# Kernel tuning notes

Measured on AMD Instinct MI355X. Metric: run time of the kernel, lower is better.

Reference implementation:

```python
import jax, jax.numpy as jnp
import numpy as np

INPUT_DIMS = 512
OUTPUT_DIMS = 512
DEGREE = 7
ALPHA = 1.0


def setup_inputs() -> dict:
    key = jax.random.key(0)
    k1, k2 = jax.random.split(key)
    x = jax.random.normal(k1, (16384, INPUT_DIMS), dtype=jnp.float32)
    std = 1.0 / (INPUT_DIMS * (DEGREE + 1))
    coeffs = jax.random.normal(k2, (INPUT_DIMS, OUTPUT_DIMS, DEGREE + 1), dtype=jnp.float32) * std
    return {"x": x, "gegenbauer_coeffs": coeffs}


def reference(x, gegenbauer_coeffs):
    # x: (B, I) -> tanh squashed into (-1, 1) domain of Gegenbauer polys
    x = jnp.tanh(x.reshape(-1, INPUT_DIMS))
    a = ALPHA
    polys = [jnp.ones_like(x)]
    if DEGREE > 0:
        polys.append(2.0 * a * x)
    # recurrence: C_{n+1} = (2(n+a) x C_n - (n+2a-1) C_{n-1}) / (n+1)
    for n in range(1, DEGREE):
        polys.append((2.0 * (n + a) * x * polys[n] - (n + 2.0 * a - 1.0) * polys[n - 1]) / (n + 1.0))
    g = jnp.stack(polys, axis=-1)  # (B, I, D+1)
    y = jnp.einsum('bid,iod->bo', g, gegenbauer_coeffs)
    return y.reshape(-1, OUTPUT_DIMS)
```

## Files before the change

kernel.cpp:

```cpp
#include <hip/hip_runtime.h>
#include <hip/hip_bf16.h>


#define I_DIM 512
#define O_DIM 512
#define NDEG 8
#define BM 128
#define BN 128
#define IPB 8
#define LSTR 72
#define KITERS (I_DIM / IPB)
#define NTHREADS 256
#define W_ELEMS (I_DIM * O_DIM * NDEG)

typedef __attribute__((ext_vector_type(8))) short s8v;
typedef __attribute__((ext_vector_type(4))) float f32x4;
typedef unsigned short u16;

__device__ __forceinline__ unsigned pack2bf(float a, float b) {
    unsigned ua = __float_as_uint(a), ub = __float_as_uint(b);
    ua += 0x7fffu + ((ua >> 16) & 1u);
    ub += 0x7fffu + ((ub >> 16) & 1u);
    return (ua >> 16) | (ub & 0xffff0000u);
}

__device__ __forceinline__ float fast_tanh(float v) {
    float e = __expf(v + v);
    float r = __builtin_amdgcn_rcpf(e + 1.0f);
    return 1.0f - (r + r);
}

extern "C" __global__ __launch_bounds__(256)
void cvt_w(const float* __restrict__ cf, u16* __restrict__ wbf) {
    const size_t idx = ((size_t)blockIdx.x * 256 + threadIdx.x) * 4;
    const float4 v = *reinterpret_cast<const float4*>(cf + idx);
    unsigned* dst = reinterpret_cast<unsigned*>(wbf + idx);
    dst[0] = pack2bf(v.x, v.y);
    dst[1] = pack2bf(v.z, v.w);
}

template <bool PRECONV>
__global__ __launch_bounds__(NTHREADS, 4)
void gegen_gemm(const float* __restrict__ x,
                const float* __restrict__ cf,
                const u16* __restrict__ wbf,
                float* __restrict__ out)
{
    __shared__ u16 As[BM * LSTR];
    __shared__ u16 Ws[IPB * BN * NDEG];

    const int tid  = threadIdx.x;
    const int lane = tid & 63;
    const int wave = tid >> 6;
    const int fm   = lane & 15;
    const int fq   = lane >> 4;
    const int wr   = (wave >> 1) << 6;
    const int wc   = (wave & 1) << 6;

    const int bm0 = blockIdx.y * BM;
    const int bn0 = blockIdx.x * BN;

    const int ar = tid >> 1;
    const int ai = (tid & 1) << 2;
    const float* xp = x + (size_t)(bm0 + ar) * I_DIM + ai;

    f32x4 acc[4][4];
#pragma unroll
    for (int a = 0; a < 4; ++a)
#pragma unroll
        for (int b = 0; b < 4; ++b)
            acc[a][b] = (f32x4){0.0f, 0.0f, 0.0f, 0.0f};

    for (int it = 0; it < KITERS; ++it) {
        if (PRECONV) {
            const u16* wsrc = wbf + ((size_t)(it * IPB) * O_DIM + bn0) * NDEG;
#pragma unroll
            for (int q = 0; q < 4; ++q) {
                const int c    = wave * 4 + q;
                const int il   = c >> 1;
                const int half = c & 1;
                const u16* src = wsrc + ((size_t)il * O_DIM + half * 64 + lane) * NDEG;
                u16* dst = &Ws[(il * BN + half * 64) * NDEG];
                __builtin_amdgcn_global_load_lds(
                    (const __attribute__((address_space(1))) void*)src,
                    (__attribute__((address_space(3))) void*)dst, 16, 0, 0);
            }
        } else {
#pragma unroll
            for (int jj = 0; jj < 4; ++jj) {
                const int p  = jj * NTHREADS + tid;
                const int il = p >> 7;
                const int o  = p & 127;
                const float* src = cf + ((size_t)(it * IPB + il) * O_DIM + bn0 + o) * NDEG;
                const float4 w0 = reinterpret_cast<const float4*>(src)[0];
                const float4 w1 = reinterpret_cast<const float4*>(src)[1];
                union { s8v s; unsigned u[4]; } pk;
                pk.u[0] = pack2bf(w0.x, w0.y);
                pk.u[1] = pack2bf(w0.z, w0.w);
                pk.u[2] = pack2bf(w1.x, w1.y);
                pk.u[3] = pack2bf(w1.z, w1.w);
                *reinterpret_cast<s8v*>(&Ws[(il * BN + o) * NDEG]) = pk.s;
            }
        }

        {
            const float4 xv = *reinterpret_cast<const float4*>(xp + it * IPB);
            const float vv[4] = {xv.x, xv.y, xv.z, xv.w};
#pragma unroll
            for (int j = 0; j < 4; ++j) {
                const float t  = fast_tanh(vv[j]);
                const float t2 = t + t;
                const float c1 = t2;
                const float c2 = t2 * c1 - 1.0f;
                const float c3 = t2 * c2 - c1;
                const float c4 = t2 * c3 - c2;
                const float c5 = t2 * c4 - c3;
                const float c6 = t2 * c5 - c4;
                const float c7 = t2 * c6 - c5;
                union { s8v s; unsigned u[4]; } pk;
                pk.u[0] = pack2bf(1.0f, c1);
                pk.u[1] = pack2bf(c2, c3);
                pk.u[2] = pack2bf(c4, c5);
                pk.u[3] = pack2bf(c6, c7);
                *reinterpret_cast<s8v*>(&As[ar * LSTR + (ai + j) * NDEG]) = pk.s;
            }
        }
        __syncthreads();

#pragma unroll
        for (int kc = 0; kc < 2; ++kc) {
            s8v afr[4], bfr[4];
#pragma unroll
            for (int tm = 0; tm < 4; ++tm)
                afr[tm] = *reinterpret_cast<const s8v*>(
                    &As[(wr + tm * 16 + fm) * LSTR + kc * 32 + fq * 8]);
#pragma unroll
            for (int tn = 0; tn < 4; ++tn)
                bfr[tn] = *reinterpret_cast<const s8v*>(
                    &Ws[((kc * 4 + fq) * BN + wc + tn * 16 + fm) * NDEG]);
#pragma unroll
            for (int tm = 0; tm < 4; ++tm)
#pragma unroll
                for (int tn = 0; tn < 4; ++tn)
                    acc[tm][tn] = __builtin_amdgcn_mfma_f32_16x16x32_bf16(
                        afr[tm], bfr[tn], acc[tm][tn], 0, 0, 0);
        }
        __syncthreads();
    }

#pragma unroll
    for (int tm = 0; tm < 4; ++tm) {
#pragma unroll
        for (int tn = 0; tn < 4; ++tn) {
            const int row = bm0 + wr + tm * 16 + fq * 4;
            const int col = bn0 + wc + tn * 16 + fm;
#pragma unroll
            for (int r = 0; r < 4; ++r)
                out[(size_t)(row + r) * O_DIM + col] = acc[tm][tn][r];
        }
    }
}

extern "C" void kernel_launch(void* const* d_in, const int* in_sizes, int n_in,
                              void* d_out, int out_size, void* d_ws, size_t ws_size,
                              hipStream_t stream) {
    const float* x  = (const float*)d_in[0];
    const float* cf = (const float*)d_in[1];
    float* out = (float*)d_out;
    const int M = in_sizes[0] / I_DIM;
    dim3 grid(O_DIM / BN, M / BM);
    dim3 block(NTHREADS, 1, 1);

    if (ws_size >= (size_t)W_ELEMS * sizeof(u16)) {
        u16* wbf = (u16*)d_ws;
        cvt_w<<<W_ELEMS / 1024, 256, 0, stream>>>(cf, wbf);
        gegen_gemm<true><<<grid, block, 0, stream>>>(x, cf, wbf, out);
    } else {
        gegen_gemm<false><<<grid, block, 0, stream>>>(x, cf, nullptr, out);
    }
}
```

Baseline: 172.2 us.

## Double-buffer LDS tiles to overlap next-tile loads with MFMA compute

Splits the A and W shared-memory tiles into two buffers and restructures the K loop so the next iteration's weight copy (async global_load_lds) and x load are issued before computing on the current buffer. The Gegenbauer polynomial generation for the next tile happens after the MFMAs, leaving one barrier per iteration instead of two. This aims to hide global-memory latency and cut synchronisation. It doubles LDS use and lowers the occupancy hint from 4 to 2 blocks per CU, which could reduce latency hiding across waves.

```diff
diff --git a/kernel.cpp b/kernel.cpp
--- a/kernel.cpp
+++ b/kernel.cpp
@@ -40,14 +40,14 @@
 }
 
 template <bool PRECONV>
-__global__ __launch_bounds__(NTHREADS, 4)
+__global__ __launch_bounds__(NTHREADS, 2)
 void gegen_gemm(const float* __restrict__ x,
                 const float* __restrict__ cf,
                 const u16* __restrict__ wbf,
                 float* __restrict__ out)
 {
-    __shared__ u16 As[BM * LSTR];
-    __shared__ u16 Ws[IPB * BN * NDEG];
+    __shared__ u16 As[2][BM * LSTR];
+    __shared__ u16 Ws[2][IPB * BN * NDEG];
 
     const int tid  = threadIdx.x;
     const int lane = tid & 63;
@@ -71,7 +71,7 @@
         for (int b = 0; b < 4; ++b)
             acc[a][b] = (f32x4){0.0f, 0.0f, 0.0f, 0.0f};
 
-    for (int it = 0; it < KITERS; ++it) {
+    auto stage_w = [&](int it, int buf) {
         if (PRECONV) {
             const u16* wsrc = wbf + ((size_t)(it * IPB) * O_DIM + bn0) * NDEG;
 #pragma unroll
@@ -80,7 +80,7 @@
                 const int il   = c >> 1;
                 const int half = c & 1;
                 const u16* src = wsrc + ((size_t)il * O_DIM + half * 64 + lane) * NDEG;
-                u16* dst = &Ws[(il * BN + half * 64) * NDEG];
+                u16* dst = &Ws[buf][(il * BN + half * 64) * NDEG];
                 __builtin_amdgcn_global_load_lds(
                     (const __attribute__((address_space(1))) void*)src,
                     (__attribute__((address_space(3))) void*)dst, 16, 0, 0);
@@ -99,45 +99,45 @@
                 pk.u[1] = pack2bf(w0.z, w0.w);
                 pk.u[2] = pack2bf(w1.x, w1.y);
                 pk.u[3] = pack2bf(w1.z, w1.w);
-                *reinterpret_cast<s8v*>(&Ws[(il * BN + o) * NDEG]) = pk.s;
+                *reinterpret_cast<s8v*>(&Ws[buf][(il * BN + o) * NDEG]) = pk.s;
             }
         }
+    };
 
-        {
-            const float4 xv = *reinterpret_cast<const float4*>(xp + it * IPB);
-            const float vv[4] = {xv.x, xv.y, xv.z, xv.w};
+    auto stage_a = [&](float4 xv, int buf) {
+        const float vv[4] = {xv.x, xv.y, xv.z, xv.w};
 #pragma unroll
-            for (int j = 0; j < 4; ++j) {
-                const float t  = fast_tanh(vv[j]);
-                const float t2 = t + t;
-                const float c1 = t2;
-                const float c2 = t2 * c1 - 1.0f;
-                const float c3 = t2 * c2 - c1;
-                const float c4 = t2 * c3 - c2;
-                const float c5 = t2 * c4 - c3;
-                const float c6 = t2 * c5 - c4;
-                const float c7 = t2 * c6 - c5;
-                union { s8v s; unsigned u[4]; } pk;
-                pk.u[0] = pack2bf(1.0f, c1);
-                pk.u[1] = pack2bf(c2, c3);
-                pk.u[2] = pack2bf(c4, c5);
-                pk.u[3] = pack2bf(c6, c7);
-                *reinterpret_cast<s8v*>(&As[ar * LSTR + (ai + j) * NDEG]) = pk.s;
-            }
+        for (int j = 0; j < 4; ++j) {
+            const float t  = fast_tanh(vv[j]);
+            const float t2 = t + t;
+            const float c1 = t2;
+            const float c2 = t2 * c1 - 1.0f;
+            const float c3 = t2 * c2 - c1;
+            const float c4 = t2 * c3 - c2;
+            const float c5 = t2 * c4 - c3;
+            const float c6 = t2 * c5 - c4;
+            const float c7 = t2 * c6 - c5;
+            union { s8v s; unsigned u[4]; } pk;
+            pk.u[0] = pack2bf(1.0f, c1);
+            pk.u[1] = pack2bf(c2, c3);
+            pk.u[2] = pack2bf(c4, c5);
+            pk.u[3] = pack2bf(c6, c7);
+            *reinterpret_cast<s8v*>(&As[buf][ar * LSTR + (ai + j) * NDEG]) = pk.s;
         }
-        __syncthreads();
+    };
 
+    auto compute = [&](int buf) {
 #pragma unroll
         for (int kc = 0; kc < 2; ++kc) {
             s8v afr[4], bfr[4];
 #pragma unroll
             for (int tm = 0; tm < 4; ++tm)
                 afr[tm] = *reinterpret_cast<const s8v*>(
-                    &As[(wr + tm * 16 + fm) * LSTR + kc * 32 + fq * 8]);
+                    &As[buf][(wr + tm * 16 + fm) * LSTR + kc * 32 + fq * 8]);
 #pragma unroll
             for (int tn = 0; tn < 4; ++tn)
                 bfr[tn] = *reinterpret_cast<const s8v*>(
-                    &Ws[((kc * 4 + fq) * BN + wc + tn * 16 + fm) * NDEG]);
+                    &Ws[buf][((kc * 4 + fq) * BN + wc + tn * 16 + fm) * NDEG]);
 #pragma unroll
             for (int tm = 0; tm < 4; ++tm)
 #pragma unroll
@@ -145,8 +145,23 @@
                     acc[tm][tn] = __builtin_amdgcn_mfma_f32_16x16x32_bf16(
                         afr[tm], bfr[tn], acc[tm][tn], 0, 0, 0);
         }
+    };
+
+    stage_w(0, 0);
+    stage_a(*reinterpret_cast<const float4*>(xp), 0);
+    __syncthreads();
+
+    int cur = 0;
+    for (int it = 0; it < KITERS - 1; ++it) {
+        const int nxt = cur ^ 1;
+        stage_w(it + 1, nxt);
+        const float4 xv = *reinterpret_cast<const float4*>(xp + (it + 1) * IPB);
+        compute(cur);
+        stage_a(xv, nxt);
         __syncthreads();
+        cur = nxt;
     }
+    compute(cur);
 
 #pragma unroll
     for (int tm = 0; tm < 4; ++tm) {
```

Result: slower. 178.8 us (+3.8%).
